# Kernel optimization log

Hardware: AMD Instinct MI355X
Metric: run time of the kernel (lower is better)

Reference implementation:

```python
import jax, jax.numpy as jnp
import numpy as np


def _run_stacked_lstm(x, init_hc, params):
    """x: [B,T,E]; init_hc: tuple of (h,c) per layer; params: tuple of (W,U,b) per layer.
    Keras LSTMCell gate order: i, f, g(candidate), o; sigmoid recurrent act, tanh act."""
    def step(carry, xt):
        inp = xt
        new = []
        for (h, c), (W, U, b) in zip(carry, params):
            z = inp @ W + h @ U + b                      # [B, 4*units]
            i, f, g, o = jnp.split(z, 4, axis=-1)
            c2 = jax.nn.sigmoid(f) * c + jax.nn.sigmoid(i) * jnp.tanh(g)
            h2 = jax.nn.sigmoid(o) * jnp.tanh(c2)
            new.append((h2, c2))
            inp = h2                                     # feed to next layer
        return tuple(new), inp
    carry, ys = jax.lax.scan(step, init_hc, jnp.swapaxes(x, 0, 1))
    return jnp.swapaxes(ys, 0, 1), carry                 # [B,T,units], final states


def setup_inputs() -> dict:
    key = jax.random.key(0)
    ks = jax.random.split(key, 20)
    B, T, V, E, H, L = 16, 64, 32000, 512, 512, 2
    s = 0.02
    inp = {
        'ids_1': jax.random.randint(ks[0], (B, T), 0, V),
        'ids_2': jax.random.randint(ks[1], (B, T), 0, V),
        'init_state': jax.random.normal(ks[2], (L, B, H), jnp.float32),
        'emb': jax.random.normal(ks[3], (V, E), jnp.float32) * s,
        'W1_0': jax.random.normal(ks[4], (E, 4 * H), jnp.float32) * s,
        'U1_0': jax.random.normal(ks[5], (H, 4 * H), jnp.float32) * s,
        'b1_0': jnp.zeros((4 * H,), jnp.float32),
        'W1_1': jax.random.normal(ks[6], (H, 4 * H), jnp.float32) * s,
        'U1_1': jax.random.normal(ks[7], (H, 4 * H), jnp.float32) * s,
        'b1_1': jnp.zeros((4 * H,), jnp.float32),
        'W2_0': jax.random.normal(ks[8], (E, 8 * H), jnp.float32) * s,
        'U2_0': jax.random.normal(ks[9], (2 * H, 8 * H), jnp.float32) * s,
        'b2_0': jnp.zeros((8 * H,), jnp.float32),
        'W2_1': jax.random.normal(ks[10], (2 * H, 8 * H), jnp.float32) * s,
        'U2_1': jax.random.normal(ks[11], (2 * H, 8 * H), jnp.float32) * s,
        'b2_1': jnp.zeros((8 * H,), jnp.float32),
        'Wp1': jax.random.normal(ks[12], (H, V), jnp.float32) * s,
        'bp1': jnp.zeros((V,), jnp.float32),
        'Wp2': jax.random.normal(ks[13], (2 * H, V), jnp.float32) * s,
        'bp2': jnp.zeros((V,), jnp.float32),
    }
    return inp


def reference(ids_1, ids_2, init_state, emb,
              W1_0, U1_0, b1_0, W1_1, U1_1, b1_1,
              W2_0, U2_0, b2_0, W2_1, U2_1, b2_1,
              Wp1, bp1, Wp2, bp2):
    L = init_state.shape[0]
    e1 = emb[ids_1]                                       # [B,T,E]
    e2 = emb[ids_2]
    # RNN1: initial (h,c) both set to init_state per layer
    init1 = tuple((init_state[l], init_state[l]) for l in range(L))
    p1 = ((W1_0, U1_0, b1_0), (W1_1, U1_1, b1_1))
    out1, st1 = _run_stacked_lstm(e1, init1, p1)
    logits1 = out1 @ Wp1 + bp1                            # [B,T,V]
    # RNN2: initial h = concat(init, h1_final), c = concat(init, c1_final)
    init2 = tuple((jnp.concatenate([init_state[l], st1[l][0]], axis=1),
                   jnp.concatenate([init_state[l], st1[l][1]], axis=1))
                  for l in range(L))
    p2 = ((W2_0, U2_0, b2_0), (W2_1, U2_1, b2_1))
    out2, _ = _run_stacked_lstm(e2, init2, p2)
    logits2 = out2 @ Wp2 + bp2                            # [B,T,V]
    return (logits1, logits2)
```

## Files before the change

kernel.cpp:

```cpp
#include <hip/hip_runtime.h>
#include <hip/hip_bf16.h>

#define B_ 16
#define T_ 64
#define E_ 512
#define H_ 512
#define V_ 32000

typedef __attribute__((ext_vector_type(4))) float f32x4;
typedef __attribute__((ext_vector_type(8))) short s16x8;

__device__ __forceinline__ float sigm(float x){ return 1.0f/(1.0f + __expf(-x)); }

__device__ __forceinline__ unsigned short f2bf(float x){
  unsigned int u = __float_as_uint(x);
  return (unsigned short)((u + 0x7FFFu + ((u>>16)&1u)) >> 16);
}

__device__ __forceinline__ unsigned load_coh(const unsigned* p){
  unsigned v;
  asm volatile("global_load_dword %0, %1, off sc0 sc1\n\ts_waitcnt vmcnt(0)"
               : "=v"(v) : "v"(p) : "memory");
  return v;
}
__device__ __forceinline__ void store_coh16(unsigned short* p, unsigned v){
  asm volatile("global_store_short %0, %1, off sc0 sc1" :: "v"(p), "v"(v) : "memory");
}
__device__ __forceinline__ void store_cohf(float* p, float v){
  asm volatile("global_store_dword %0, %1, off sc0 sc1" :: "v"(p), "v"(v) : "memory");
}
__device__ __forceinline__ void store_cohu(unsigned* p, unsigned v){
  asm volatile("global_store_dword %0, %1, off sc0 sc1" :: "v"(p), "v"(v) : "memory");
}

__device__ __forceinline__ void gbar3(unsigned* barb, unsigned bi1, int nblk, bool det){
  asm volatile("s_waitcnt vmcnt(0)" ::: "memory");
  __syncthreads();
  const int tid = threadIdx.x;
  unsigned* gen = barb + 4096;
  if(tid == 0) store_cohu(barb + (size_t)blockIdx.x*16, bi1);
  if(det){
    if(tid < nblk){
      const unsigned* fp = barb + (size_t)tid*16;
      while(load_coh(fp) < bi1) __builtin_amdgcn_s_sleep(1);
    }
    __syncthreads();
    if(tid == 0) store_cohu(gen, bi1);
  } else {
    if(tid == 0){
      while(load_coh(gen) < bi1) __builtin_amdgcn_s_sleep(1);
    }
  }
  __syncthreads();
}

__global__ void k_barinit(unsigned* bar){
  int i = blockIdx.x*256 + threadIdx.x;
  if(i < 16384) bar[i] = 0u;
}

__global__ void k_gather(const int* __restrict__ ids, const float* __restrict__ emb,
                         unsigned short* __restrict__ out){
  const int row = blockIdx.x;
  const int id  = ids[row];
  float4 v = *(const float4*)(emb + (size_t)id*E_ + threadIdx.x*4);
  ushort4 o;
  o.x = f2bf(v.x); o.y = f2bf(v.y); o.z = f2bf(v.z); o.w = f2bf(v.w);
  *(ushort4*)(out + (size_t)row*E_ + threadIdx.x*4) = o;
}

__global__ __launch_bounds__(256)
void k_tcvt(const float* __restrict__ in, unsigned short* __restrict__ out,
            int N, int Hp, int Kfull, int koff, int swz){
  __shared__ float tile[32][33];
  const int n0 = blockIdx.x*32, k0 = blockIdx.y*32;
  const int x = threadIdx.x & 31, y = threadIdx.x >> 5;
  #pragma unroll
  for(int i=0;i<4;i++){
    int k = y + i*8;
    tile[k][x] = in[(size_t)(k0+k)*N + n0 + x];
  }
  __syncthreads();
  #pragma unroll
  for(int i=0;i<4;i++){
    int nl = y + i*8;
    int n  = n0 + nl;
    int p  = Hp ? ((n % Hp)*4 + n / Hp) : n;
    int kk = koff + k0 + x;
    size_t idx;
    if(swz){
      int k2 = kk*2;
      int slot = ((k2>>4)&7) ^ (p&7);
      idx = (size_t)p*Kfull + (((k2 & ~127) | (slot<<4) | (k2 & 15)) >> 1);
    } else {
      idx = (size_t)p*Kfull + kk;
    }
    out[idx] = f2bf(tile[x][nl]);
  }
}

__global__ void k_bpack(const float* __restrict__ b, float* __restrict__ out, int H, int N){
  int p = blockIdx.x*256 + threadIdx.x;
  if(p < N) out[p] = b[(p&3)*H + (p>>2)];
}

__global__ void k_init1(const float* __restrict__ init_state,
                        unsigned short* h0i, float* c0i, unsigned short* h1i, float* c1i){
  int i = blockIdx.x*256 + threadIdx.x;
  if(i >= B_*H_) return;
  float v0 = init_state[i];
  float v1 = init_state[B_*H_ + i];
  h0i[i] = f2bf(v0); c0i[i] = v0;
  h1i[i] = f2bf(v1); c1i[i] = v1;
}

__global__ void k_init2(const float* __restrict__ init_state,
                        const unsigned short* __restrict__ h0seq1,
                        const unsigned short* __restrict__ h1seq1,
                        const float* __restrict__ c0f1, const float* __restrict__ c1f1,
                        unsigned short* h20i, unsigned short* h21i,
                        float* c20i, float* c21i){
  const int l = blockIdx.y;
  int i = blockIdx.x*256 + threadIdx.x;
  if(i >= B_*2*H_) return;
  const int r = i >> 10, j = i & 1023;
  unsigned short* ho = l ? h21i : h20i;
  float* co = l ? c21i : c20i;
  if(j < H_){
    float v = init_state[(size_t)l*B_*H_ + r*H_ + j];
    ho[i] = f2bf(v); co[i] = v;
  } else {
    const unsigned short* hs = l ? h1seq1 : h0seq1;
    const float* cf = l ? c1f1 : c0f1;
    ho[i] = hs[(size_t)(r*T_ + (T_-1))*H_ + (j - H_)];
    co[i] = cf[r*H_ + (j - H_)];
  }
}

template<int BF32>
__global__ __launch_bounds__(256)
void k_mm(const unsigned short* __restrict__ A, const void* __restrict__ Bsrc,
          const float* __restrict__ bias, float* __restrict__ C,
          int M, int N, int K){
  __shared__ __align__(16) unsigned short As[128*64];
  __shared__ __align__(16) unsigned short Bs[128*64];
  const int tid = threadIdx.x;
  const int lane = tid & 63, w = tid >> 6;
  const int wm = (w>>1)*64, wn = (w&1)*64;
  const int bm = blockIdx.y*128, bn = blockIdx.x*128;
  const int l15 = lane & 15, kg = lane >> 4;
  f32x4 acc[4][4] = {};

  for(int k0=0; k0<K; k0+=64){
    __syncthreads();
    #pragma unroll
    for(int ch=0; ch<4; ch++){
      int off = ch*4096 + tid*16;
      int row = off >> 7;
      int s   = ((off >> 4) & 7) ^ (row & 7);
      __builtin_amdgcn_global_load_lds(
        (const __attribute__((address_space(1))) unsigned int*)(A + (size_t)(bm+row)*K + k0 + s*8),
        (__attribute__((address_space(3))) unsigned int*)((char*)As + off), 16, 0, 0);
    }
    if(BF32){
      const float* Bf = (const float*)Bsrc;
      #pragma unroll
      for(int i=0;i<8;i++){
        int kl = (tid>>5) + i*8;
        int nl = (tid&31)*4;
        float4 v = *(const float4*)(Bf + (size_t)(k0+kl)*N + bn + nl);
        int slot = kl >> 3, kb = kl & 7;
        float vv[4] = {v.x, v.y, v.z, v.w};
        #pragma unroll
        for(int jj=0;jj<4;jj++){
          int n = nl + jj;
          Bs[n*64 + ((slot ^ (n&7))*8) + kb] = f2bf(vv[jj]);
        }
      }
    } else {
      const unsigned short* Bt = (const unsigned short*)Bsrc;
      #pragma unroll
      for(int ch=0; ch<4; ch++){
        int off = ch*4096 + tid*16;
        int row = off >> 7;
        int s   = ((off >> 4) & 7) ^ (row & 7);
        __builtin_amdgcn_global_load_lds(
          (const __attribute__((address_space(1))) unsigned int*)(Bt + (size_t)(bn+row)*K + k0 + s*8),
          (__attribute__((address_space(3))) unsigned int*)((char*)Bs + off), 16, 0, 0);
      }
    }
    __syncthreads();

    #pragma unroll
    for(int q=0;q<2;q++){
      s16x8 af[4], bf[4];
      #pragma unroll
      for(int mt=0;mt<4;mt++){
        int row = wm + mt*16 + l15;
        int s = (q*4 + kg) ^ (row & 7);
        af[mt] = *(const s16x8*)(As + row*64 + s*8);
      }
      #pragma unroll
      for(int nt=0;nt<4;nt++){
        int row = wn + nt*16 + l15;
        int s = (q*4 + kg) ^ (row & 7);
        bf[nt] = *(const s16x8*)(Bs + row*64 + s*8);
      }
      #pragma unroll
      for(int mt=0;mt<4;mt++)
        #pragma unroll
        for(int nt=0;nt<4;nt++)
          acc[mt][nt] = __builtin_amdgcn_mfma_f32_16x16x32_bf16(af[mt], bf[nt], acc[mt][nt], 0, 0, 0);
    }
  }
  #pragma unroll
  for(int mt=0;mt<4;mt++){
    #pragma unroll
    for(int nt=0;nt<4;nt++){
      int col = bn + wn + nt*16 + l15;
      float bv = bias ? bias[col] : 0.f;
      #pragma unroll
      for(int e=0;e<4;e++){
        int row = bm + wm + mt*16 + kg*4 + e;
        C[(size_t)row*N + col] = acc[mt][nt][e] + bv;
      }
    }
  }
}

template<int C, int K, int LAYER, int HU>
__device__ __forceinline__ void rnn_body(
    unsigned short* __restrict__ Uld, float* __restrict__ zp,
    const unsigned short* __restrict__ Uslice,
    const float* __restrict__ xw0, const float* __restrict__ bpk,
    const unsigned short* __restrict__ h0init, const unsigned short* __restrict__ h1init,
    const float* __restrict__ cinit,
    unsigned short* __restrict__ h0seq, unsigned short* __restrict__ h1seq,
    float* __restrict__ cfin, unsigned* bar, int cb, int nblk, bool det)
{
  constexpr int KW = K/4, KS = KW/32, FR = C/16, UB = C/4;
  constexpr int K2 = K*2;
  constexpr int ITEMS = 16*UB;
  const int tid = threadIdx.x;
  const int lane = tid & 63, w = tid >> 6;
  const int l15 = lane & 15, kg = lane >> 4;

  constexpr int CP = (C*K2)/4096;
  #pragma unroll
  for(int i=0;i<CP;i++){
    __builtin_amdgcn_global_load_lds(
      (const __attribute__((address_space(1))) unsigned int*)((const char*)Uslice + i*4096 + tid*16),
      (__attribute__((address_space(3))) unsigned int*)((char*)Uld + i*4096 + tid*16), 16, 0, 0);
  }
  const int base_p = cb*C;
  const int base_u = cb*UB;
  float4 bvr = make_float4(0.f,0.f,0.f,0.f);
  int er = 0, eu = 0;
  if(tid < ITEMS){ er = tid / UB; eu = tid - er*UB; bvr = *(const float4*)(bpk + base_p + eu*4); }
  float creg = 0.f;
  unsigned short* hseqW = LAYER ? h1seq : h0seq;

  int cbyte[FR], cx[FR];
  #pragma unroll
  for(int f=0;f<FR;f++){ int c = f*16 + l15; cbyte[f] = c*K2; cx[f] = (c&7)<<4; }

  __syncthreads();

  for(int it = 0; it <= T_; ++it){
    const bool active = LAYER ? (it >= 1) : (it < T_);
    const int t = LAYER ? it-1 : it;
    if(active){
      const unsigned short* asrc;
      if constexpr(LAYER == 0){
        asrc = (t == 0) ? (h0init + l15*HU)
                        : (h0seq + ((size_t)(l15*T_ + (t-1)))*HU);
      } else {
        if(w < 2){
          asrc = h0seq + ((size_t)(l15*T_ + t))*HU;
        } else {
          asrc = ((t == 0) ? (h1init + l15*HU)
                           : (h1seq + ((size_t)(l15*T_ + (t-1)))*HU)) - HU;
        }
      }
      f32x4 acc[FR];
      #pragma unroll
      for(int f=0;f<FR;f++) acc[f] = (f32x4){0.f,0.f,0.f,0.f};
      #pragma unroll
      for(int s=0;s<KS;s++){
        const int kel = w*KW + s*32 + kg*8;
        s16x8 a = *(const s16x8*)(asrc + kel);
        const int kb  = kel*2;
        const int kch = kb & ~127;
        const int ksl = (kb >> 4) & 7;
        #pragma unroll
        for(int f=0;f<FR;f++){
          const int ad = cbyte[f] + kch + ((ksl<<4) ^ cx[f]);
          s16x8 b = *(const s16x8*)((const char*)Uld + ad);
          acc[f] = __builtin_amdgcn_mfma_f32_16x16x32_bf16(a, b, acc[f], 0, 0, 0);
        }
      }
      #pragma unroll
      for(int f=0;f<FR;f++)
        #pragma unroll
        for(int e=0;e<4;e++)
          zp[(w*16 + kg*4 + e)*68 + f*16 + l15] = acc[f][e];
    }
    __syncthreads();
    if(active && tid < ITEMS){
      float4 z0 = *(const float4*)(zp + (     er)*68 + eu*4);
      float4 z1 = *(const float4*)(zp + (16 + er)*68 + eu*4);
      float4 z2 = *(const float4*)(zp + (32 + er)*68 + eu*4);
      float4 z3 = *(const float4*)(zp + (48 + er)*68 + eu*4);
      float si = z0.x+z1.x+z2.x+z3.x + bvr.x;
      float sf = z0.y+z1.y+z2.y+z3.y + bvr.y;
      float sg = z0.z+z1.z+z2.z+z3.z + bvr.z;
      float so = z0.w+z1.w+z2.w+z3.w + bvr.w;
      if constexpr(LAYER == 0){
        float4 xv = *(const float4*)(xw0 + ((size_t)(er*T_ + t))*(4*HU) + base_p + eu*4);
        si += xv.x; sf += xv.y; sg += xv.z; so += xv.w;
      }
      float cin = (t == 0) ? cinit[er*HU + base_u + eu] : creg;
      float c2 = sigm(sf)*cin + sigm(si)*tanhf(sg);
      float h2 = sigm(so)*tanhf(c2);
      creg = c2;
      store_coh16(&hseqW[((size_t)(er*T_ + t))*HU + base_u + eu], (unsigned)f2bf(h2));
      if(t == T_-1) store_cohf(&cfin[er*HU + base_u + eu], c2);
    }
    if(it < T_) gbar3(bar, (unsigned)(it+1), nblk, det);
  }
}

template<int HU, int C0, int C1>
__global__ __launch_bounds__(256, 1)
void k_rnn(const unsigned short* __restrict__ Ut0, const unsigned short* __restrict__ WU1,
           const float* __restrict__ xw0, const float* __restrict__ bpk0, const float* __restrict__ bpk1,
           const unsigned short* __restrict__ h0init, const unsigned short* __restrict__ h1init,
           const float* __restrict__ c0init, const float* __restrict__ c1init,
           unsigned short* __restrict__ h0seq, unsigned short* __restrict__ h1seq,
           float* __restrict__ c0fin, float* __restrict__ c1fin, unsigned* bar)
{
  constexpr int NB0 = 4*HU/C0;
  constexpr int UMAXE = (C0*HU > C1*2*HU) ? C0*HU : C1*2*HU;
  __shared__ __align__(16) unsigned short Uld[UMAXE];
  __shared__ __align__(16) float zred[64*68];
  const int nblk = gridDim.x;
  const bool det = (blockIdx.x == 0);
  const int blk = blockIdx.x;
  if(blk < NB0)
    rnn_body<C0, HU, 0, HU>(Uld, zred, Ut0 + (size_t)blk*C0*HU, xw0, bpk0,
                            h0init, h1init, c0init, h0seq, h1seq, c0fin, bar, blk, nblk, det);
  else
    rnn_body<C1, 2*HU, 1, HU>(Uld, zred, WU1 + (size_t)(blk-NB0)*C1*2*HU, nullptr, bpk1,
                            h0init, h1init, c1init, h0seq, h1seq, c1fin, bar, blk-NB0, nblk, det);
}

extern "C" void kernel_launch(void* const* d_in, const int* in_sizes, int n_in,
                              void* d_out, int out_size, void* d_ws, size_t ws_size,
                              hipStream_t stream){
  const int*   ids1 = (const int*)d_in[0];
  const int*   ids2 = (const int*)d_in[1];
  const float* init = (const float*)d_in[2];
  const float* emb  = (const float*)d_in[3];
  const float* W1_0 = (const float*)d_in[4];
  const float* U1_0 = (const float*)d_in[5];
  const float* b1_0 = (const float*)d_in[6];
  const float* W1_1 = (const float*)d_in[7];
  const float* U1_1 = (const float*)d_in[8];
  const float* b1_1 = (const float*)d_in[9];
  const float* W2_0 = (const float*)d_in[10];
  const float* U2_0 = (const float*)d_in[11];
  const float* b2_0 = (const float*)d_in[12];
  const float* W2_1 = (const float*)d_in[13];
  const float* U2_1 = (const float*)d_in[14];
  const float* b2_1 = (const float*)d_in[15];
  const float* Wp1  = (const float*)d_in[16];
  const float* bp1  = (const float*)d_in[17];
  const float* Wp2  = (const float*)d_in[18];
  const float* bp2  = (const float*)d_in[19];
  float* out1 = (float*)d_out;
  float* out2 = out1 + (size_t)B_*T_*V_;

  char* base = (char*)d_ws;
  float*          xw    = (float*)(base);
  unsigned short* ut0_1 = (unsigned short*)(base + (16u<<20));
  unsigned short* wu1_1 = (unsigned short*)(base + (18u<<20));
  unsigned short* ut0_2 = (unsigned short*)(base + (22u<<20));
  unsigned short* wu1_2 = (unsigned short*)(base + (30u<<20));
  unsigned short* wtmp  = (unsigned short*)(base + (46u<<20));
  unsigned short* ebuf  = (unsigned short*)(base + (50u<<20));
  unsigned short* h0s1  = (unsigned short*)(base + (51u<<20));
  unsigned short* h1s1  = (unsigned short*)(base + (52u<<20));
  unsigned short* h0s2  = (unsigned short*)(base + (53u<<20));
  unsigned short* h1s2  = (unsigned short*)(base + (55u<<20));
  char* M = base + (57u<<20);
  unsigned short* h0i1 = (unsigned short*)(M);
  unsigned short* h1i1 = (unsigned short*)(M + 16384);
  float* c0i1 = (float*)(M + 32768);
  float* c1i1 = (float*)(M + 65536);
  unsigned short* h2i0 = (unsigned short*)(M + 98304);
  unsigned short* h2i1 = (unsigned short*)(M + 131072);
  float* c2i0 = (float*)(M + 163840);
  float* c2i1 = (float*)(M + 229376);
  float* c0f1 = (float*)(M + 294912);
  float* c1f1 = (float*)(M + 327680);
  float* c0f2 = (float*)(M + 360448);
  float* c1f2 = (float*)(M + 425984);
  float* bpk10 = (float*)(M + 491520);
  float* bpk11 = (float*)(M + 499712);
  float* bpk20 = (float*)(M + 507904);
  float* bpk21 = (float*)(M + 524288);
  unsigned* bar1 = (unsigned*)(M + 540672);
  unsigned* bar2 = (unsigned*)(M + 540672 + 32768);
  unsigned short* wpT = (unsigned short*)(base + (58u<<20));
  const size_t NEED_ALL = ((size_t)58u<<20) + (size_t)V_*1024*2;
  const bool wide = ws_size >= NEED_ALL;

  k_barinit<<<dim3(64), dim3(256), 0, stream>>>(bar1);

  k_init1<<<dim3(32), dim3(256), 0, stream>>>(init, h0i1, c0i1, h1i1, c1i1);
  k_gather<<<dim3(B_*T_), dim3(128), 0, stream>>>(ids1, emb, ebuf);
  k_tcvt<<<dim3(64, 16), dim3(256), 0, stream>>>(U1_0, ut0_1, 2048, 512, 512, 0, 1);
  k_tcvt<<<dim3(64, 16), dim3(256), 0, stream>>>(W1_0, wtmp,  2048, 512, 512, 0, 0);
  k_tcvt<<<dim3(64, 16), dim3(256), 0, stream>>>(W1_1, wu1_1, 2048, 512, 1024, 0, 1);
  k_tcvt<<<dim3(64, 16), dim3(256), 0, stream>>>(U1_1, wu1_1, 2048, 512, 1024, 512, 1);
  k_bpack<<<dim3(8),  dim3(256), 0, stream>>>(b1_0, bpk10, 512, 2048);
  k_bpack<<<dim3(8),  dim3(256), 0, stream>>>(b1_1, bpk11, 512, 2048);
  k_mm<0><<<dim3(16, 8), dim3(256), 0, stream>>>(ebuf, wtmp, nullptr, xw, 1024, 2048, 512);
  k_rnn<512, 64, 64><<<dim3(64), dim3(256), 0, stream>>>(ut0_1, wu1_1, xw, bpk10, bpk11,
      h0i1, h1i1, c0i1, c1i1, h0s1, h1s1, c0f1, c1f1, bar1);
  if(wide){
    k_tcvt<<<dim3(1000, 16), dim3(256), 0, stream>>>(Wp1, wpT, V_, 0, 512, 0, 0);
    k_mm<0><<<dim3(250, 8), dim3(256), 0, stream>>>(h1s1, wpT, bp1, out1, 1024, V_, 512);
  } else {
    k_mm<1><<<dim3(250, 8), dim3(256), 0, stream>>>(h1s1, Wp1, bp1, out1, 1024, V_, 512);
  }

  k_init2<<<dim3(64, 2), dim3(256), 0, stream>>>(init, h0s1, h1s1, c0f1, c1f1,
                                                 h2i0, h2i1, c2i0, c2i1);
  k_gather<<<dim3(B_*T_), dim3(128), 0, stream>>>(ids2, emb, ebuf);
  k_tcvt<<<dim3(128, 32), dim3(256), 0, stream>>>(U2_0, ut0_2, 4096, 1024, 1024, 0, 1);
  k_tcvt<<<dim3(128, 16), dim3(256), 0, stream>>>(W2_0, wtmp,  4096, 1024, 512, 0, 0);
  k_tcvt<<<dim3(128, 32), dim3(256), 0, stream>>>(W2_1, wu1_2, 4096, 1024, 2048, 0, 1);
  k_tcvt<<<dim3(128, 32), dim3(256), 0, stream>>>(U2_1, wu1_2, 4096, 1024, 2048, 1024, 1);
  k_bpack<<<dim3(16), dim3(256), 0, stream>>>(b2_0, bpk20, 1024, 4096);
  k_bpack<<<dim3(16), dim3(256), 0, stream>>>(b2_1, bpk21, 1024, 4096);
  k_mm<0><<<dim3(32, 8), dim3(256), 0, stream>>>(ebuf, wtmp, nullptr, xw, 1024, 4096, 512);
  k_rnn<1024, 64, 32><<<dim3(192), dim3(256), 0, stream>>>(ut0_2, wu1_2, xw, bpk20, bpk21,
      h2i0, h2i1, c2i0, c2i1, h0s2, h1s2, c0f2, c1f2, bar2);
  if(wide){
    k_tcvt<<<dim3(1000, 32), dim3(256), 0, stream>>>(Wp2, wpT, V_, 0, 1024, 0, 0);
    k_mm<0><<<dim3(250, 8), dim3(256), 0, stream>>>(h1s2, wpT, bp2, out2, 1024, V_, 1024);
  } else {
    k_mm<1><<<dim3(250, 8), dim3(256), 0, stream>>>(h1s2, Wp2, bp2, out2, 1024, V_, 1024);
  }
}
```

Measured before the change: 907.5 us.

## Overlap RNN recurrences with weight prep and projection GEMMs on idle blocks

The recurrent kernels now launch 256 blocks: the RNN blocks run the sequential LSTM recurrence while the spare blocks do independent work. During RNN1 they gather the second embedding, pack biases and transpose-convert the RNN2 weights and Wp1. During RNN2 they run the logits1 GEMM and the Wp2 transpose. The global barrier release flag is also spread over 8 cache lines so waiting blocks poll different addresses. This hides preprocessing and projection work behind latency-bound recurrences, but the extra traffic may slow the barrier-sensitive RNN steps and it needs a larger workspace.

```diff
diff --git a/kernel.cpp b/kernel.cpp
--- a/kernel.cpp
+++ b/kernel.cpp
@@ -33,22 +33,23 @@
   asm volatile("global_store_dword %0, %1, off sc0 sc1" :: "v"(p), "v"(v) : "memory");
 }
 
-__device__ __forceinline__ void gbar3(unsigned* barb, unsigned bi1, int nblk, bool det){
+__device__ __forceinline__ void gbar3(unsigned* barb, unsigned bi1, int nblk,
+                                      bool det, int myblk){
   asm volatile("s_waitcnt vmcnt(0)" ::: "memory");
   __syncthreads();
   const int tid = threadIdx.x;
-  unsigned* gen = barb + 4096;
-  if(tid == 0) store_cohu(barb + (size_t)blockIdx.x*16, bi1);
+  if(tid == 0) store_cohu(barb + (size_t)myblk*16, bi1);
   if(det){
     if(tid < nblk){
       const unsigned* fp = barb + (size_t)tid*16;
       while(load_coh(fp) < bi1) __builtin_amdgcn_s_sleep(1);
     }
     __syncthreads();
-    if(tid == 0) store_cohu(gen, bi1);
+    if(tid < 8) store_cohu(barb + 4096 + (size_t)tid*16, bi1);
   } else {
     if(tid == 0){
-      while(load_coh(gen) < bi1) __builtin_amdgcn_s_sleep(1);
+      const unsigned* gp = barb + 4096 + (size_t)(myblk & 7)*16;
+      while(load_coh(gp) < bi1) __builtin_amdgcn_s_sleep(1);
     }
   }
   __syncthreads();
@@ -69,12 +70,12 @@
   *(ushort4*)(out + (size_t)row*E_ + threadIdx.x*4) = o;
 }
 
-__global__ __launch_bounds__(256)
-void k_tcvt(const float* __restrict__ in, unsigned short* __restrict__ out,
-            int N, int Hp, int Kfull, int koff, int swz){
-  __shared__ float tile[32][33];
-  const int n0 = blockIdx.x*32, k0 = blockIdx.y*32;
+__device__ __forceinline__ void tcvt_dev(const float* __restrict__ in,
+    unsigned short* __restrict__ out, int N, int Hp, int Kfull, int koff, int swz,
+    int bx, int by, float (*tile)[33]){
+  const int n0 = bx*32, k0 = by*32;
   const int x = threadIdx.x & 31, y = threadIdx.x >> 5;
+  __syncthreads();
   #pragma unroll
   for(int i=0;i<4;i++){
     int k = y + i*8;
@@ -97,6 +98,13 @@
     }
     out[idx] = f2bf(tile[x][nl]);
   }
+}
+
+__global__ __launch_bounds__(256)
+void k_tcvt(const float* __restrict__ in, unsigned short* __restrict__ out,
+            int N, int Hp, int Kfull, int koff, int swz){
+  __shared__ float tile[32][33];
+  tcvt_dev(in, out, N, Hp, Kfull, koff, swz, blockIdx.x, blockIdx.y, tile);
 }
 
 __global__ void k_bpack(const float* __restrict__ b, float* __restrict__ out, int H, int N){
@@ -137,6 +145,73 @@
   }
 }
 
+__device__ __forceinline__ void mm_tile(const unsigned short* __restrict__ A,
+    const unsigned short* __restrict__ Bt, const float* __restrict__ bias,
+    float* __restrict__ C, int N, int K, int bm, int bn,
+    unsigned short* As, unsigned short* Bs){
+  const int tid = threadIdx.x;
+  const int lane = tid & 63, w = tid >> 6;
+  const int wm = (w>>1)*64, wn = (w&1)*64;
+  const int l15 = lane & 15, kg = lane >> 4;
+  f32x4 acc[4][4] = {};
+  for(int k0=0; k0<K; k0+=64){
+    __syncthreads();
+    #pragma unroll
+    for(int ch=0; ch<4; ch++){
+      int off = ch*4096 + tid*16;
+      int row = off >> 7;
+      int s   = ((off >> 4) & 7) ^ (row & 7);
+      __builtin_amdgcn_global_load_lds(
+        (const __attribute__((address_space(1))) unsigned int*)(A + (size_t)(bm+row)*K + k0 + s*8),
+        (__attribute__((address_space(3))) unsigned int*)((char*)As + off), 16, 0, 0);
+    }
+    #pragma unroll
+    for(int ch=0; ch<4; ch++){
+      int off = ch*4096 + tid*16;
+      int row = off >> 7;
+      int s   = ((off >> 4) & 7) ^ (row & 7);
+      __builtin_amdgcn_global_load_lds(
+        (const __attribute__((address_space(1))) unsigned int*)(Bt + (size_t)(bn+row)*K + k0 + s*8),
+        (__attribute__((address_space(3))) unsigned int*)((char*)Bs + off), 16, 0, 0);
+    }
+    __syncthreads();
+    #pragma unroll
+    for(int q=0;q<2;q++){
+      s16x8 af[4], bf[4];
+      #pragma unroll
+      for(int mt=0;mt<4;mt++){
+        int row = wm + mt*16 + l15;
+        int s = (q*4 + kg) ^ (row & 7);
+        af[mt] = *(const s16x8*)(As + row*64 + s*8);
+      }
+      #pragma unroll
+      for(int nt=0;nt<4;nt++){
+        int row = wn + nt*16 + l15;
+        int s = (q*4 + kg) ^ (row & 7);
+        bf[nt] = *(const s16x8*)(Bs + row*64 + s*8);
+      }
+      #pragma unroll
+      for(int mt=0;mt<4;mt++)
+        #pragma unroll
+        for(int nt=0;nt<4;nt++)
+          acc[mt][nt] = __builtin_amdgcn_mfma_f32_16x16x32_bf16(af[mt], bf[nt], acc[mt][nt], 0, 0, 0);
+    }
+  }
+  #pragma unroll
+  for(int mt=0;mt<4;mt++){
+    #pragma unroll
+    for(int nt=0;nt<4;nt++){
+      int col = bn + wn + nt*16 + l15;
+      float bv = bias ? bias[col] : 0.f;
+      #pragma unroll
+      for(int e=0;e<4;e++){
+        int row = bm + wm + mt*16 + kg*4 + e;
+        C[(size_t)row*N + col] = acc[mt][nt][e] + bv;
+      }
+    }
+  }
+}
+
 template<int BF32>
 __global__ __launch_bounds__(256)
 void k_mm(const unsigned short* __restrict__ A, const void* __restrict__ Bsrc,
@@ -144,13 +219,17 @@
           int M, int N, int K){
   __shared__ __align__(16) unsigned short As[128*64];
   __shared__ __align__(16) unsigned short Bs[128*64];
+  if(!BF32){
+    mm_tile(A, (const unsigned short*)Bsrc, bias, C, N, K,
+            blockIdx.y*128, blockIdx.x*128, As, Bs);
+    return;
+  }
   const int tid = threadIdx.x;
   const int lane = tid & 63, w = tid >> 6;
   const int wm = (w>>1)*64, wn = (w&1)*64;
   const int bm = blockIdx.y*128, bn = blockIdx.x*128;
   const int l15 = lane & 15, kg = lane >> 4;
   f32x4 acc[4][4] = {};
-
   for(int k0=0; k0<K; k0+=64){
     __syncthreads();
     #pragma unroll
@@ -162,7 +241,7 @@
         (const __attribute__((address_space(1))) unsigned int*)(A + (size_t)(bm+row)*K + k0 + s*8),
         (__attribute__((address_space(3))) unsigned int*)((char*)As + off), 16, 0, 0);
     }
-    if(BF32){
+    {
       const float* Bf = (const float*)Bsrc;
       #pragma unroll
       for(int i=0;i<8;i++){
@@ -177,20 +256,8 @@
           Bs[n*64 + ((slot ^ (n&7))*8) + kb] = f2bf(vv[jj]);
         }
       }
-    } else {
-      const unsigned short* Bt = (const unsigned short*)Bsrc;
-      #pragma unroll
-      for(int ch=0; ch<4; ch++){
-        int off = ch*4096 + tid*16;
-        int row = off >> 7;
-        int s   = ((off >> 4) & 7) ^ (row & 7);
-        __builtin_amdgcn_global_load_lds(
-          (const __attribute__((address_space(1))) unsigned int*)(Bt + (size_t)(bn+row)*K + k0 + s*8),
-          (__attribute__((address_space(3))) unsigned int*)((char*)Bs + off), 16, 0, 0);
-      }
     }
     __syncthreads();
-
     #pragma unroll
     for(int q=0;q<2;q++){
       s16x8 af[4], bf[4];
@@ -236,7 +303,7 @@
     const unsigned short* __restrict__ h0init, const unsigned short* __restrict__ h1init,
     const float* __restrict__ cinit,
     unsigned short* __restrict__ h0seq, unsigned short* __restrict__ h1seq,
-    float* __restrict__ cfin, unsigned* bar, int cb, int nblk, bool det)
+    float* __restrict__ cfin, unsigned* bar, int cb, int nblk, bool det, int myblk)
 {
   constexpr int KW = K/4, KS = KW/32, FR = C/16, UB = C/4;
   constexpr int K2 = K*2;
@@ -326,32 +393,105 @@
       store_coh16(&hseqW[((size_t)(er*T_ + t))*HU + base_u + eu], (unsigned)f2bf(h2));
       if(t == T_-1) store_cohf(&cfin[er*HU + base_u + eu], c2);
     }
-    if(it < T_) gbar3(bar, (unsigned)(it+1), nblk, det);
-  }
-}
-
-template<int HU, int C0, int C1>
+    if(it < T_) gbar3(bar, (unsigned)(it+1), nblk, det, myblk);
+  }
+}
+
 __global__ __launch_bounds__(256, 1)
-void k_rnn(const unsigned short* __restrict__ Ut0, const unsigned short* __restrict__ WU1,
-           const float* __restrict__ xw0, const float* __restrict__ bpk0, const float* __restrict__ bpk1,
-           const unsigned short* __restrict__ h0init, const unsigned short* __restrict__ h1init,
-           const float* __restrict__ c0init, const float* __restrict__ c1init,
-           unsigned short* __restrict__ h0seq, unsigned short* __restrict__ h1seq,
-           float* __restrict__ c0fin, float* __restrict__ c1fin, unsigned* bar)
+void k_rnn1m(const unsigned short* __restrict__ Ut0, const unsigned short* __restrict__ WU1,
+    const float* __restrict__ xw0, const float* __restrict__ bpk0, const float* __restrict__ bpk1,
+    const unsigned short* __restrict__ h0init, const unsigned short* __restrict__ h1init,
+    const float* __restrict__ c0init, const float* __restrict__ c1init,
+    unsigned short* __restrict__ h0seq, unsigned short* __restrict__ h1seq,
+    float* __restrict__ c0fin, float* __restrict__ c1fin, unsigned* bar,
+    const int* __restrict__ ids2, const float* __restrict__ emb, unsigned short* __restrict__ ebuf2,
+    const float* __restrict__ b2_0, const float* __restrict__ b2_1,
+    float* __restrict__ bpk20, float* __restrict__ bpk21,
+    const float* __restrict__ U2_0, unsigned short* __restrict__ ut0_2,
+    const float* __restrict__ W2_0, unsigned short* __restrict__ wtmp2,
+    const float* __restrict__ W2_1, const float* __restrict__ U2_1, unsigned short* __restrict__ wu1_2,
+    const float* __restrict__ Wp1, unsigned short* __restrict__ wpT1, int wide)
 {
+  constexpr int HU = 512, C0 = 64, C1 = 64;
   constexpr int NB0 = 4*HU/C0;
-  constexpr int UMAXE = (C0*HU > C1*2*HU) ? C0*HU : C1*2*HU;
-  __shared__ __align__(16) unsigned short Uld[UMAXE];
+  constexpr int NRNN = NB0 + 4*HU/C1;
+  __shared__ __align__(16) unsigned short Uld[65536];
   __shared__ __align__(16) float zred[64*68];
-  const int nblk = gridDim.x;
-  const bool det = (blockIdx.x == 0);
   const int blk = blockIdx.x;
-  if(blk < NB0)
+  if(blk < NB0){
     rnn_body<C0, HU, 0, HU>(Uld, zred, Ut0 + (size_t)blk*C0*HU, xw0, bpk0,
-                            h0init, h1init, c0init, h0seq, h1seq, c0fin, bar, blk, nblk, det);
-  else
+        h0init, h1init, c0init, h0seq, h1seq, c0fin, bar, blk, NRNN, blk==0, blk);
+  } else if(blk < NRNN){
     rnn_body<C1, 2*HU, 1, HU>(Uld, zred, WU1 + (size_t)(blk-NB0)*C1*2*HU, nullptr, bpk1,
-                            h0init, h1init, c1init, h0seq, h1seq, c1fin, bar, blk-NB0, nblk, det);
+        h0init, h1init, c1init, h0seq, h1seq, c1fin, bar, blk-NB0, NRNN, false, blk);
+  } else {
+    const int q = blk - NRNN;
+    const int NQ = 256 - NRNN;
+    float (*tile)[33] = (float(*)[33])Uld;
+    const int tid = threadIdx.x;
+    const int J0 = 512, J1 = J0+32, J2 = J1+4096, J3 = J2+2048, J4 = J3+4096, J5 = J4+4096;
+    const int totJ = wide ? (J5 + 16000) : J5;
+    for(int j = q; j < totJ; j += NQ){
+      if(j < J0){
+        int row = j*2 + (tid>>7);
+        int id = ids2[row];
+        float4 v = *(const float4*)(emb + (size_t)id*E_ + (tid&127)*4);
+        ushort4 o; o.x=f2bf(v.x); o.y=f2bf(v.y); o.z=f2bf(v.z); o.w=f2bf(v.w);
+        *(ushort4*)(ebuf2 + (size_t)row*E_ + (tid&127)*4) = o;
+      } else if(j < J1){
+        int jj = j - J0;
+        const float* b = (jj < 16) ? b2_0 : b2_1;
+        float* o = (jj < 16) ? bpk20 : bpk21;
+        int p = (jj & 15)*256 + tid;
+        o[p] = b[(p&3)*1024 + (p>>2)];
+      } else if(j < J2){
+        int r = j - J1; tcvt_dev(U2_0, ut0_2, 4096, 1024, 1024, 0, 1, r%128, r/128, tile);
+      } else if(j < J3){
+        int r = j - J2; tcvt_dev(W2_0, wtmp2, 4096, 1024, 512, 0, 0, r%128, r/128, tile);
+      } else if(j < J4){
+        int r = j - J3; tcvt_dev(W2_1, wu1_2, 4096, 1024, 2048, 0, 1, r%128, r/128, tile);
+      } else if(j < J5){
+        int r = j - J4; tcvt_dev(U2_1, wu1_2, 4096, 1024, 2048, 1024, 1, r%128, r/128, tile);
+      } else {
+        int r = j - J5; tcvt_dev(Wp1, wpT1, 32000, 0, 512, 0, 0, r%1000, r/1000, tile);
+      }
+    }
+  }
+}
+
+__global__ __launch_bounds__(256, 1)
+void k_rnn2m(const unsigned short* __restrict__ Ut0, const unsigned short* __restrict__ WU1,
+    const float* __restrict__ xw0, const float* __restrict__ bpk0, const float* __restrict__ bpk1,
+    const unsigned short* __restrict__ h0init, const unsigned short* __restrict__ h1init,
+    const float* __restrict__ c0init, const float* __restrict__ c1init,
+    unsigned short* __restrict__ h0seq, unsigned short* __restrict__ h1seq,
+    float* __restrict__ c0fin, float* __restrict__ c1fin, unsigned* bar,
+    const unsigned short* __restrict__ h1s1, const unsigned short* __restrict__ wpT1,
+    const float* __restrict__ bp1, float* __restrict__ out1,
+    const float* __restrict__ Wp2, unsigned short* __restrict__ wpT2, int wide)
+{
+  constexpr int HU = 1024, C0 = 64, C1 = 32;
+  constexpr int NB0 = 4*HU/C0;
+  constexpr int NRNN = NB0 + 4*HU/C1;
+  __shared__ __align__(16) unsigned short Uld[65536];
+  __shared__ __align__(16) float zred[64*68];
+  const int blk = blockIdx.x;
+  if(blk < NB0){
+    rnn_body<C0, HU, 0, HU>(Uld, zred, Ut0 + (size_t)blk*C0*HU, xw0, bpk0,
+        h0init, h1init, c0init, h0seq, h1seq, c0fin, bar, blk, NRNN, blk==0, blk);
+  } else if(blk < NRNN){
+    rnn_body<C1, 2*HU, 1, HU>(Uld, zred, WU1 + (size_t)(blk-NB0)*C1*2*HU, nullptr, bpk1,
+        h0init, h1init, c1init, h0seq, h1seq, c1fin, bar, blk-NB0, NRNN, false, blk);
+  } else if(wide){
+    const int q = blk - NRNN;
+    unsigned short* As = Uld;
+    unsigned short* Bs = Uld + 128*64;
+    for(int t = q; t < 2000; t += 64)
+      mm_tile(h1s1, wpT1, bp1, out1, V_, 512, (t/250)*128, (t%250)*128, As, Bs);
+    float (*tile)[33] = (float(*)[33])Uld;
+    for(int t = q; t < 32000; t += 64)
+      tcvt_dev(Wp2, wpT2, 32000, 0, 1024, 0, 0, t%1000, t/1000, tile);
+  }
 }
 
 extern "C" void kernel_launch(void* const* d_in, const int* in_sizes, int n_in,
@@ -411,8 +551,9 @@
   float* bpk21 = (float*)(M + 524288);
   unsigned* bar1 = (unsigned*)(M + 540672);
   unsigned* bar2 = (unsigned*)(M + 540672 + 32768);
-  unsigned short* wpT = (unsigned short*)(base + (58u<<20));
-  const size_t NEED_ALL = ((size_t)58u<<20) + (size_t)V_*1024*2;
+  unsigned short* wpT1 = (unsigned short*)(base + (58u<<20));
+  unsigned short* wpT2 = (unsigned short*)(base + (90u<<20));
+  const size_t NEED_ALL = ((size_t)90u<<20) + (size_t)V_*1024*2;
   const bool wide = ws_size >= NEED_ALL;
 
   k_barinit<<<dim3(64), dim3(256), 0, stream>>>(bar1);
@@ -426,30 +567,25 @@
   k_bpack<<<dim3(8),  dim3(256), 0, stream>>>(b1_0, bpk10, 512, 2048);
   k_bpack<<<dim3(8),  dim3(256), 0, stream>>>(b1_1, bpk11, 512, 2048);
   k_mm<0><<<dim3(16, 8), dim3(256), 0, stream>>>(ebuf, wtmp, nullptr, xw, 1024, 2048, 512);
-  k_rnn<512, 64, 64><<<dim3(64), dim3(256), 0, stream>>>(ut0_1, wu1_1, xw, bpk10, bpk11,
-      h0i1, h1i1, c0i1, c1i1, h0s1, h1s1, c0f1, c1f1, bar1);
-  if(wide){
-    k_tcvt<<<dim3(1000, 16), dim3(256), 0, stream>>>(Wp1, wpT, V_, 0, 512, 0, 0);
-    k_mm<0><<<dim3(250, 8), dim3(256), 0, stream>>>(h1s1, wpT, bp1, out1, 1024, V_, 512);
-  } else {
-    k_mm<1><<<dim3(250, 8), dim3(256), 0, stream>>>(h1s1, Wp1, bp1, out1, 1024, V_, 512);
-  }
-
+
+  k_rnn1m<<<dim3(256), dim3(256), 0, stream>>>(ut0_1, wu1_1, xw, bpk10, bpk11,
+      h0i1, h1i1, c0i1, c1i1, h0s1, h1s1, c0f1, c1f1, bar1,
+      ids2, emb, ebuf, b2_0, b2_1, bpk20, bpk21,
+      U2_0, ut0_2, W2_0, wtmp, W2_1, U2_1, wu1_2, Wp1, wpT1, (int)wide);
+
+  k_mm<0><<<dim3(32, 8), dim3(256), 0, stream>>>(ebuf, wtmp, nullptr, xw, 1024, 4096, 512);
   k_init2<<<dim3(64, 2), dim3(256), 0, stream>>>(init, h0s1, h1s1, c0f1, c1f1,
                                                  h2i0, h2i1, c2i0, c2i1);
-  k_gather<<<dim3(B_*T_), dim3(128), 0, stream>>>(ids2, emb, ebuf);
-  k_tcvt<<<dim3(128, 32), dim3(256), 0, stream>>>(U2_0, ut0_2, 4096, 1024, 1024, 0, 1);
-  k_tcvt<<<dim3(128, 16), dim3(256), 0, stream>>>(W2_0, wtmp,  4096, 1024, 512, 0, 0);
-  k_tcvt<<<dim3(128, 32), dim3(256), 0, stream>>>(W2_1, wu1_2, 4096, 1024, 2048, 0, 1);
-  k_tcvt<<<dim3(128, 32), dim3(256), 0, stream>>>(U2_1, wu1_2, 4096, 1024, 2048, 1024, 1);
-  k_bpack<<<dim3(16), dim3(256), 0, stream>>>(b2_0, bpk20, 1024, 4096);
-  k_bpack<<<dim3(16), dim3(256), 0, stream>>>(b2_1, bpk21, 1024, 4096);
-  k_mm<0><<<dim3(32, 8), dim3(256), 0, stream>>>(ebuf, wtmp, nullptr, xw, 1024, 4096, 512);
-  k_rnn<1024, 64, 32><<<dim3(192), dim3(256), 0, stream>>>(ut0_2, wu1_2, xw, bpk20, bpk21,
-      h2i0, h2i1, c2i0, c2i1, h0s2, h1s2, c0f2, c1f2, bar2);
+  if(!wide){
+    k_mm<1><<<dim3(250, 8), dim3(256), 0, stream>>>(h1s1, Wp1, bp1, out1, 1024, V_, 512);
+  }
+
+  k_rnn2m<<<dim3(256), dim3(256), 0, stream>>>(ut0_2, wu1_2, xw, bpk20, bpk21,
+      h2i0, h2i1, c2i0, c2i1, h0s2, h1s2, c0f2, c1f2, bar2,
+      h1s1, wpT1, bp1, out1, Wp2, wpT2, (int)wide);
+
   if(wide){
-    k_tcvt<<<dim3(1000, 32), dim3(256), 0, stream>>>(Wp2, wpT, V_, 0, 1024, 0, 0);
-    k_mm<0><<<dim3(250, 8), dim3(256), 0, stream>>>(h1s2, wpT, bp2, out2, 1024, V_, 1024);
+    k_mm<0><<<dim3(250, 8), dim3(256), 0, stream>>>(h1s2, wpT2, bp2, out2, 1024, V_, 1024);
   } else {
     k_mm<1><<<dim3(250, 8), dim3(256), 0, stream>>>(h1s2, Wp2, bp2, out2, 1024, V_, 1024);
   }
```

New measurement: 1.136 ms. 25.2% more time.
